# Kernel tuning notes

Hardware: AMD Instinct MI355X
Metric: run time of the kernel (lower is better)

## Reference

```python
import jax, jax.numpy as jnp
import numpy as np

D_MODEL = 768
N_LAYER = 8
EXPAND = 2
D_INNER = EXPAND * D_MODEL          # 1536
HEADDIM = 64
NHEADS = D_INNER // HEADDIM         # 24
D_STATE = 128
D_CONV = 4
NGROUPS = 1
CONV_DIM = D_INNER + 2 * NGROUPS * D_STATE      # 1792
D_IN_PROJ = 2 * D_INNER + 2 * NGROUPS * D_STATE + NHEADS  # 3352
DIM_INP = 6
DIM_OUT = 5
BATCH = 4
SEQ = 2048
EPS = 1e-5


def rmsnorm(x, w):
    return x * jax.lax.rsqrt(jnp.mean(x * x, axis=-1, keepdims=True) + EPS) * w


def setup_inputs() -> dict:
    key = jax.random.key(0)
    ks = jax.random.split(key, 12)
    nrm = lambda k, shape, s=0.02: jax.random.normal(k, shape, jnp.float32) * s
    x = jax.random.normal(ks[0], (BATCH, SEQ, DIM_INP), jnp.float32)
    y = jax.random.normal(ks[1], (BATCH, SEQ, DIM_OUT), jnp.float32)
    W_emb = nrm(ks[2], (D_MODEL, DIM_INP))
    b_emb = jnp.zeros((D_MODEL,), jnp.float32)
    # stacked per-layer Mamba2 params
    W_in = nrm(ks[3], (N_LAYER, D_IN_PROJ, D_MODEL))
    conv_w = nrm(ks[4], (N_LAYER, CONV_DIM, D_CONV), 0.2)
    conv_b = jnp.zeros((N_LAYER, CONV_DIM), jnp.float32)
    dt0 = jax.random.uniform(ks[5], (N_LAYER, NHEADS), jnp.float32, 1e-3, 1e-1)
    dt_bias = jnp.log(jnp.expm1(dt0))  # inverse softplus of target dt
    A_log = jnp.log(jax.random.uniform(ks[6], (N_LAYER, NHEADS), jnp.float32, 1.0, 16.0))
    Dp = jnp.ones((N_LAYER, NHEADS), jnp.float32)
    norm_w = jnp.ones((N_LAYER, D_INNER), jnp.float32)     # gated RMSNorm inside Mamba2
    W_out = nrm(ks[7], (N_LAYER, D_MODEL, D_INNER))
    block_norm_w = jnp.ones((N_LAYER, D_MODEL), jnp.float32)  # prenorm RMSNorm per block
    norm_f_w = jnp.ones((D_MODEL,), jnp.float32)
    W_head = nrm(ks[8], (DIM_OUT, D_MODEL))
    return dict(x=x, y=y, W_emb=W_emb, b_emb=b_emb, W_in=W_in, conv_w=conv_w,
                conv_b=conv_b, dt_bias=dt_bias, A_log=A_log, Dp=Dp, norm_w=norm_w,
                W_out=W_out, block_norm_w=block_norm_w, norm_f_w=norm_f_w, W_head=W_head)


def _mamba2(u, W_in_l, conv_w_l, conv_b_l, dt_bias_l, A_log_l, D_l, norm_w_l, W_out_l):
    B, L, _ = u.shape
    zxbcdt = jnp.einsum('bld,ed->ble', u, W_in_l)  # [B,L,D_IN_PROJ]
    z = zxbcdt[..., :D_INNER]
    xBC = zxbcdt[..., D_INNER:D_INNER + CONV_DIM]
    dt = jax.nn.softplus(zxbcdt[..., D_INNER + CONV_DIM:] + dt_bias_l)  # [B,L,H]
    # causal depthwise conv1d, kernel D_CONV
    xp = jnp.pad(xBC, ((0, 0), (D_CONV - 1, 0), (0, 0)))
    xBC = sum(xp[:, k:k + L, :] * conv_w_l[:, k] for k in range(D_CONV)) + conv_b_l
    xBC = jax.nn.silu(xBC)
    xh = xBC[..., :D_INNER].reshape(B, L, NHEADS, HEADDIM)
    Bm = xBC[..., D_INNER:D_INNER + D_STATE]   # [B,L,N] (ngroups=1)
    Cm = xBC[..., D_INNER + D_STATE:]          # [B,L,N]
    A = -jnp.exp(A_log_l)                       # [H]
    decay = jnp.exp(dt * A)                     # [B,L,H]
    dtx = dt[..., None] * xh                    # [B,L,H,P]

    def step(h, inp):
        dec_t, dtx_t, B_t, C_t = inp            # [B,H],[B,H,P],[B,N],[B,N]
        h = h * dec_t[..., None, None] + dtx_t[..., None] * B_t[:, None, None, :]
        y_t = jnp.einsum('bhpn,bn->bhp', h, C_t)
        return h, y_t

    h0 = jnp.zeros((B, NHEADS, HEADDIM, D_STATE), u.dtype)
    _, ys = jax.lax.scan(step, h0, (decay.transpose(1, 0, 2), dtx.transpose(1, 0, 2, 3),
                                    Bm.transpose(1, 0, 2), Cm.transpose(1, 0, 2)))
    ys = ys.transpose(1, 0, 2, 3) + xh * D_l[None, None, :, None]  # skip term D*x
    yf = ys.reshape(B, L, D_INNER)
    yf = rmsnorm(yf * jax.nn.silu(z), norm_w_l)  # gated RMSNorm (norm_before_gate=False)
    return jnp.einsum('bld,ed->ble', yf, W_out_l)


def _forward(x, W_emb, b_emb, W_in, conv_w, conv_b, dt_bias, A_log, Dp, norm_w,
             W_out, block_norm_w, norm_f_w, W_head):
    h = jnp.einsum('bli,di->bld', x, W_emb) + b_emb
    res = jnp.zeros_like(h)

    def layer_step(carry, lp):
        h, res = carry
        Wi, cw, cb, dtb, Al, Dl, nw, Wo, bnw = lp
        res = h + res
        hn = rmsnorm(res, bnw)
        h = _mamba2(hn, Wi, cw, cb, dtb, Al, Dl, nw, Wo)
        return (h, res), None

    (h, res), _ = jax.lax.scan(layer_step, (h, res),
                               (W_in, conv_w, conv_b, dt_bias, A_log, Dp, norm_w, W_out, block_norm_w))
    res = h + res
    hn = rmsnorm(res, norm_f_w)
    return jnp.einsum('bld,od->blo', hn, W_head)


def reference(x, y, W_emb, b_emb, W_in, conv_w, conv_b, dt_bias, A_log, Dp, norm_w,
              W_out, block_norm_w, norm_f_w, W_head):
    out = _forward(x, W_emb, b_emb, W_in, conv_w, conv_b, dt_bias, A_log, Dp, norm_w,
                   W_out, block_norm_w, norm_f_w, W_head)
    loss = jnp.mean((out - y) ** 2)
    return out, loss
```

## Files before the change

### kernel.cpp

```cpp
#include <hip/hip_runtime.h>
#include <hip/hip_bf16.h>
#include <math.h>

#define BATCH 4
#define SEQ 2048
#define DMODEL 768
#define NLAYER 8
#define DINNER 1536
#define HEADDIM 64
#define NHEADS 24
#define DSTATE 128
#define CONVDIM 1792
#define DINPROJ 3352
#define NPAD 3456
#define NPADW 3584
#define ROWS (BATCH*SEQ)
#define EPS 1e-5f
#define QCH 128
#define NCH (SEQ/QCH)

typedef __bf16 bf16;
typedef bf16 bf16x8 __attribute__((ext_vector_type(8)));
typedef bf16 bf16x4 __attribute__((ext_vector_type(4)));
typedef float f32x4 __attribute__((ext_vector_type(4)));

#define GLD(src, dst) __builtin_amdgcn_global_load_lds( \
    (const __attribute__((address_space(1))) void*)(src), \
    (__attribute__((address_space(3))) void*)(dst), 16, 0, 0)

__device__ __forceinline__ void bar_sync() {
    asm volatile("" ::: "memory");
    __builtin_amdgcn_s_barrier();
    asm volatile("" ::: "memory");
}

__device__ __forceinline__ float fsilu(float x) { return x / (1.f + __expf(-x)); }

__global__ void k_embed(const float* __restrict__ x, const float* __restrict__ We,
                        const float* __restrict__ be, float* __restrict__ res) {
    int idx = blockIdx.x * 256 + threadIdx.x;
    int d = idx % DMODEL; int bl = idx / DMODEL;
    float acc = be[d];
#pragma unroll
    for (int i = 0; i < 6; ++i) acc += x[bl * 6 + i] * We[d * 6 + i];
    res[idx] = acc;
}

__global__ __launch_bounds__(256) void k_rmsnorm(const float* __restrict__ res,
                                                 const float* __restrict__ w,
                                                 bf16* __restrict__ out) {
    __shared__ float sm[4];
    int r = blockIdx.x, tid = threadIdx.x;
    float v[3]; float ss = 0.f;
#pragma unroll
    for (int k = 0; k < 3; ++k) {
        int d = tid + k * 256;
        float t = res[r * DMODEL + d];
        v[k] = t; ss += t * t;
    }
#pragma unroll
    for (int off = 32; off; off >>= 1) ss += __shfl_down(ss, off, 64);
    if ((tid & 63) == 0) sm[tid >> 6] = ss;
    __syncthreads();
    float tot = sm[0] + sm[1] + sm[2] + sm[3];
    float sc = rsqrtf(tot / (float)DMODEL + EPS);
#pragma unroll
    for (int k = 0; k < 3; ++k) {
        int d = tid + k * 256;
        out[r * DMODEL + d] = (bf16)(v[k] * sc * w[d]);
    }
}

__global__ void k_cvt_in(const float* __restrict__ src, bf16* __restrict__ dst) {
    int idx = blockIdx.x * 256 + threadIdx.x;
    int l = idx / (NPADW * DMODEL);
    int rem = idx % (NPADW * DMODEL);
    int n = rem / DMODEL;
    int d = rem % DMODEL;
    dst[idx] = (n < DINPROJ) ? (bf16)src[(long)l * DINPROJ * DMODEL + n * DMODEL + d] : (bf16)0.f;
}
__global__ void k_cvt_out(const float* __restrict__ src, bf16* __restrict__ dst) {
    int idx = blockIdx.x * 256 + threadIdx.x;
    dst[idx] = (bf16)src[idx];
}

template <typename OT, int BM, int BN, int TH, bool ACC>
__global__ __launch_bounds__(TH) void k_gemm(const bf16* __restrict__ A, const bf16* __restrict__ B,
                                             OT* __restrict__ C, int K, int ldc, int Nact) {
    constexpr int NW  = TH / 64;
    constexpr int nWn = (BN / 64 < 4) ? BN / 64 : 4;
    constexpr int nWm = NW / nWn;
    constexpr int WMR = BM / nWm;
    constexpr int MI  = WMR / 16;
    constexpr int NI  = 4;
    constexpr int RG  = TH / 8;
    constexpr int AG  = BM / RG;
    constexpr int BG  = BN / RG;
    __shared__ bf16 As[2][BM * 64];
    __shared__ bf16 Bs[2][BN * 64];
    const int tid = threadIdx.x;
    const int lane = tid & 63;
    const int w = tid >> 6;
    const int wm = w / nWn, wn = w % nWn;
    const long rowA0 = (long)blockIdx.x * BM;
    const long rowB0 = (long)blockIdx.y * BN;
    const int srow = tid >> 3;
    const int scol = ((tid & 7) ^ (srow & 7)) * 8;
    const bf16* Ab = A + rowA0 * K + scol;
    const bf16* Bb = B + rowB0 * K + scol;

    f32x4 acc[MI][NI];
    const f32x4 vz = {0.f, 0.f, 0.f, 0.f};
#pragma unroll
    for (int mi = 0; mi < MI; ++mi)
#pragma unroll
        for (int ni = 0; ni < NI; ++ni) acc[mi][ni] = vz;

    auto stage = [&](int buf, int kt) {
#pragma unroll
        for (int j = 0; j < AG; ++j)
            GLD(Ab + (long)(j * RG + srow) * K + kt, &As[buf][(j * TH + w * 64) * 8]);
#pragma unroll
        for (int j = 0; j < BG; ++j)
            GLD(Bb + (long)(j * RG + srow) * K + kt, &Bs[buf][(j * TH + w * 64) * 8]);
    };
    auto waitv = [&]() {
        if constexpr (AG + BG == 8) asm volatile("s_waitcnt vmcnt(8)" ::: "memory");
        else                        asm volatile("s_waitcnt vmcnt(6)" ::: "memory");
    };
    auto compute = [&](int buf) {
        const char* AsB = (const char*)As[buf];
        const char* BsB = (const char*)Bs[buf];
#pragma unroll
        for (int s = 0; s < 2; ++s) {
            bf16x8 af[MI], bfr[NI];
#pragma unroll
            for (int mi = 0; mi < MI; ++mi) {
                int r = wm * WMR + mi * 16 + (lane & 15);
                af[mi] = *(const bf16x8*)(AsB + r * 128 + ((s * 64 + (lane >> 4) * 16) ^ ((r & 7) << 4)));
            }
#pragma unroll
            for (int ni = 0; ni < NI; ++ni) {
                int r = wn * 64 + ni * 16 + (lane & 15);
                bfr[ni] = *(const bf16x8*)(BsB + r * 128 + ((s * 64 + (lane >> 4) * 16) ^ ((r & 7) << 4)));
            }
#pragma unroll
            for (int mi = 0; mi < MI; ++mi)
#pragma unroll
                for (int ni = 0; ni < NI; ++ni)
                    acc[mi][ni] = __builtin_amdgcn_mfma_f32_16x16x32_bf16(af[mi], bfr[ni], acc[mi][ni], 0, 0, 0);
        }
    };

    stage(0, 0);
    stage(1, 64);
    int cur = 0;
    for (int kt = 128; kt < K; kt += 64) {
        waitv();
        bar_sync();
        compute(cur);
        bar_sync();
        stage(cur, kt);
        cur ^= 1;
    }
    waitv();
    bar_sync();
    compute(cur);
    asm volatile("s_waitcnt vmcnt(0)" ::: "memory");
    bar_sync();
    compute(cur ^ 1);

    const int crow = (lane >> 4) * 4;
    const int ccol = lane & 15;
#pragma unroll
    for (int mi = 0; mi < MI; ++mi)
#pragma unroll
        for (int ni = 0; ni < NI; ++ni) {
            long r0 = rowA0 + wm * WMR + mi * 16 + crow;
            long c0 = rowB0 + wn * 64 + ni * 16 + ccol;
            if ((int)c0 < Nact) {
#pragma unroll
                for (int j = 0; j < 4; ++j) {
                    if constexpr (ACC) C[(r0 + j) * ldc + c0] += (OT)acc[mi][ni][j];
                    else               C[(r0 + j) * ldc + c0]  = (OT)acc[mi][ni][j];
                }
            }
        }
}

__global__ void k_convBC(const bf16* __restrict__ zx, const float* __restrict__ cw,
                         const float* __restrict__ cb, bf16* __restrict__ bc) {
    int idx = blockIdx.x * 256 + threadIdx.x;
    int c8 = idx & 31; int blt = idx >> 5;
    int t = blt % SEQ;
    int ch = DINNER + c8 * 8;
    long bbase = (long)(blt - t) * NPAD;
    float cwa[8][4];
#pragma unroll
    for (int j = 0; j < 8; ++j) {
        float4 tv = *(const float4*)(cw + (ch + j) * 4);
        cwa[j][0] = tv.x; cwa[j][1] = tv.y; cwa[j][2] = tv.z; cwa[j][3] = tv.w;
    }
    float acc[8];
#pragma unroll
    for (int j = 0; j < 8; ++j) acc[j] = cb[ch + j];
#pragma unroll
    for (int k = 0; k < 4; ++k) {
        int tt = t + k - 3;
        if (tt >= 0) {
            bf16x8 v = *(const bf16x8*)(zx + bbase + (long)tt * NPAD + DINNER + ch);
#pragma unroll
            for (int j = 0; j < 8; ++j) acc[j] += (float)v[j] * cwa[j][k];
        }
    }
    bf16x8 o;
#pragma unroll
    for (int j = 0; j < 8; ++j) o[j] = (bf16)fsilu(acc[j]);
    *(bf16x8*)(bc + (long)blt * 256 + c8 * 8) = o;
}

__global__ __launch_bounds__(256) void k_prepL(const bf16* __restrict__ zx, const bf16* __restrict__ bc,
                                               const float* __restrict__ cw_l, const float* __restrict__ cb_l,
                                               const float* __restrict__ dt_bias_l,
                                               const float* __restrict__ Alog,
                                               float* __restrict__ Sarr, float* __restrict__ dtc,
                                               float* __restrict__ Pcb,
                                               bf16* __restrict__ XT, bf16* __restrict__ Lbuf) {
    __shared__ float S_lds[128], wl_lds[128], wtot[2];
    __shared__ bf16 Xs[136 * 64];
    __shared__ bf16 Xw[64 * 128];
    __shared__ bf16 Bt[128 * 128];
    int blk = blockIdx.x;
    int b = blk / (NHEADS * NCH);
    int r = blk % (NHEADS * NCH);
    int h = r / NCH;
    int c = r % NCH;
    int tid = threadIdx.x, lane = tid & 63, wid = tid >> 6;
    long brow0 = (long)b * SEQ + c * QCH;
#pragma unroll
    for (int i = 0; i < 5; ++i) {
        int base = i * 256 + wid * 64;
        if (base < 1048) {
            int idx = base + lane;
            long g = brow0 - 3 + (idx >> 3);
            if (g < 0) g = 0;
            if (g > (long)ROWS - 1) g = (long)ROWS - 1;
            GLD(zx + g * NPAD + DINNER + h * HEADDIM + (idx & 7) * 8,
                (char*)Xs + (long)base * 16);
        }
    }
    float ps = 0.f, dtv = 0.f;
    if (tid < 128) {
        float raw = (float)zx[(brow0 + tid) * NPAD + DINNER + CONVDIM + h] + dt_bias_l[h];
        dtv = (raw > 15.f) ? raw : log1pf(__expf(raw));
        float Ah = -__expf(Alog[h]);
        ps = dtv * Ah;
#pragma unroll
        for (int off = 1; off < 64; off <<= 1) {
            float o = __shfl_up(ps, off, 64);
            if ((tid & 63) >= off) ps += o;
        }
        if ((tid & 63) == 63) wtot[tid >> 6] = ps;
    }
    __syncthreads();
    if (tid < 128) {
        if (tid >= 64) ps += wtot[0];
        S_lds[tid] = ps;
    }
    __syncthreads();
    float Sl = S_lds[127];
    if (tid < 128) {
        wl_lds[tid] = __expf(Sl - ps) * dtv;
        Sarr[blk * QCH + tid] = ps;
        dtc[blk * QCH + tid] = dtv;
        if (tid == 127) Pcb[blk] = __expf(Sl);
    }
    __syncthreads();
    {
        int p = tid >> 2, q = tid & 3;
        float4 cwv = *(const float4*)(cw_l + (h * HEADDIM + p) * 4);
        float cbv = cb_l[h * HEADDIM + p];
        float cwa[4] = {cwv.x, cwv.y, cwv.z, cwv.w};
        char* xtb = (char*)XT + (((long)blk) << 14);
#pragma unroll
        for (int ub = 0; ub < 4; ++ub) {
            int u0 = q * 32 + ub * 8;
            bf16x8 vx, vw;
#pragma unroll
            for (int k = 0; k < 8; ++k) {
                int u = u0 + k;
                float a = cbv;
#pragma unroll
                for (int tt = 0; tt < 4; ++tt) {
                    if (c > 0 || u + tt >= 3)
                        a += (float)Xs[(u + tt) * 64 + p] * cwa[tt];
                }
                bf16 xb = (bf16)fsilu(a);
                vx[k] = xb;
                vw[k] = (bf16)((float)xb * wl_lds[u]);
            }
            long off = (long)((p * 256 + u0 * 2) ^ ((p & 7) << 4));
            *(bf16x8*)(xtb + off) = vx;
            *(bf16x8*)((char*)Xw + off) = vw;
        }
    }
#pragma unroll
    for (int nb = 0; nb < 2; ++nb) {
        __syncthreads();
#pragma unroll
        for (int i = 0; i < 4; ++i) {
            int idx = i * 256 + tid;
            GLD(bc + (brow0 + (idx >> 3)) * 256 + nb * 64 + (idx & 7) * 8,
                (char*)Xs + (i * 256 + wid * 64) * 16);
        }
        __syncthreads();
        int nl = tid >> 2, q = tid & 3;
        int n = nb * 64 + nl;
#pragma unroll
        for (int ub = 0; ub < 4; ++ub) {
            int u0 = q * 32 + ub * 8;
            bf16x8 v;
#pragma unroll
            for (int k = 0; k < 8; ++k) v[k] = Xs[(u0 + k) * 64 + nl];
            long off = (long)((n * 256 + u0 * 2) ^ ((n & 7) << 4));
            *(bf16x8*)((char*)Bt + off) = v;
        }
    }
    __syncthreads();
    f32x4 acc[4][2];
    const f32x4 vz = {0.f, 0.f, 0.f, 0.f};
#pragma unroll
    for (int mi = 0; mi < 4; ++mi)
#pragma unroll
        for (int ni = 0; ni < 2; ++ni) acc[mi][ni] = vz;
    const char* XwB = (const char*)Xw;
    const char* BtB = (const char*)Bt;
    __builtin_amdgcn_s_setprio(1);
#pragma unroll
    for (int ks = 0; ks < 4; ++ks) {
        bf16x8 af[4], bfr[2];
#pragma unroll
        for (int mi = 0; mi < 4; ++mi) {
            int pp = mi * 16 + (lane & 15);
            af[mi] = *(const bf16x8*)(XwB + ((pp * 256 + ks * 64 + (lane >> 4) * 16) ^ ((pp & 7) << 4)));
        }
#pragma unroll
        for (int ni = 0; ni < 2; ++ni) {
            int n = wid * 32 + ni * 16 + (lane & 15);
            bfr[ni] = *(const bf16x8*)(BtB + ((n * 256 + ks * 64 + (lane >> 4) * 16) ^ ((n & 7) << 4)));
        }
#pragma unroll
        for (int mi = 0; mi < 4; ++mi)
#pragma unroll
            for (int ni = 0; ni < 2; ++ni)
                acc[mi][ni] = __builtin_amdgcn_mfma_f32_16x16x32_bf16(af[mi], bfr[ni], acc[mi][ni], 0, 0, 0);
    }
    __builtin_amdgcn_s_setprio(0);
    char* lb = (char*)Lbuf + (((long)blk) << 14);
#pragma unroll
    for (int mi = 0; mi < 4; ++mi)
#pragma unroll
        for (int ni = 0; ni < 2; ++ni)
#pragma unroll
            for (int j = 0; j < 4; ++j) {
                int pp = mi * 16 + (lane >> 4) * 4 + j;
                int n = wid * 32 + ni * 16 + (lane & 15);
                *(bf16*)(lb + ((pp * 256 + n * 2) ^ ((pp & 7) << 4))) = (bf16)acc[mi][ni][j];
            }
}

__global__ __launch_bounds__(256) void k_scanB(bf16* __restrict__ Lbuf, const float* __restrict__ Pc) {
    int bh = blockIdx.x >> 2;
    int q = blockIdx.x & 3;
    int off = (q * 256 + threadIdx.x) * 8;
    long base = ((long)bh * NCH) << 13;
    float s[8] = {0.f};
#pragma unroll
    for (int c = 0; c < NCH; ++c) {
        bf16* p = Lbuf + base + ((long)c << 13) + off;
        bf16x8 L = *(bf16x8*)p;
        bf16x8 I;
#pragma unroll
        for (int k = 0; k < 8; ++k) I[k] = (bf16)s[k];
        float P = Pc[bh * NCH + c];
#pragma unroll
        for (int k = 0; k < 8; ++k) s[k] = P * s[k] + (float)L[k];
        *(bf16x8*)p = I;
    }
}

__global__ __launch_bounds__(512) void k_chunkY(const bf16* __restrict__ bc,
                                                const float* __restrict__ Sarr, const float* __restrict__ dtc,
                                                const float* __restrict__ Dp,
                                                const bf16* __restrict__ XT, const bf16* __restrict__ Lbuf,
                                                bf16* __restrict__ ysb) {
    __shared__ bf16 Cs[128 * 128];
    __shared__ bf16 Bs[128 * 128];
    __shared__ bf16 Xts[64 * 128];
    __shared__ bf16 Is[64 * 128];
    __shared__ float S_lds[128], dt_lds[128];
    int blk = blockIdx.x;
    int b = blk / (NHEADS * NCH);
    int r = blk % (NHEADS * NCH);
    int h = r / NCH;
    int c = r % NCH;
    int tid = threadIdx.x, lane = tid & 63, wid = tid >> 6;
    long brow0 = (long)b * SEQ + c * QCH;
    const char* bcB = (const char*)bc;
#pragma unroll
    for (int i = 0; i < 4; ++i) {
        int trow = i * 32 + wid * 4 + (lane >> 4);
        int blk16 = lane & 15;
        const char* rp = bcB + (brow0 + trow) * 512;
        int sb = (blk16 ^ (trow & 7)) << 4;
        GLD(rp + 256 + sb, (char*)Cs + (i * 32 + wid * 4) * 256);
        GLD(rp + sb,       (char*)Bs + (i * 32 + wid * 4) * 256);
    }
    const char* xt = (const char*)XT + (((long)blk) << 14);
    const char* ib = (const char*)Lbuf + (((long)blk) << 14);
#pragma unroll
    for (int i = 0; i < 2; ++i) {
        GLD(xt + (long)(i * 512 + tid) * 16, (char*)Xts + (i * 512 + wid * 64) * 16);
        GLD(ib + (long)(i * 512 + tid) * 16, (char*)Is + (i * 512 + wid * 64) * 16);
    }
    if (tid < 128) { S_lds[tid] = Sarr[blk * QCH + tid]; dt_lds[tid] = dtc[blk * QCH + tid]; }
    float Dh = Dp[h];
    asm volatile("s_waitcnt vmcnt(4) lgkmcnt(0)" ::: "memory");
    bar_sync();
    const char* CsB = (const char*)Cs;
    char* BsB = (char*)Bs;
    const char* IsB = (const char*)Is;
    const char* XtB = (const char*)Xts;
    const f32x4 vz = {0.f, 0.f, 0.f, 0.f};
    int wmG = wid >> 2, wnG = wid & 3;
    f32x4 accg[4][2];
#pragma unroll
    for (int mi = 0; mi < 4; ++mi)
#pragma unroll
        for (int ni = 0; ni < 2; ++ni) accg[mi][ni] = vz;
#pragma unroll
    for (int ks = 0; ks < 4; ++ks) {
        bf16x8 af[4], bfr[2];
#pragma unroll
        for (int mi = 0; mi < 4; ++mi) {
            int t = wmG * 64 + mi * 16 + (lane & 15);
            af[mi] = *(const bf16x8*)(CsB + ((t * 256 + ks * 64 + (lane >> 4) * 16) ^ ((t & 7) << 4)));
        }
#pragma unroll
        for (int ni = 0; ni < 2; ++ni) {
            int u = wnG * 32 + ni * 16 + (lane & 15);
            bfr[ni] = *(const bf16x8*)(BsB + ((u * 256 + ks * 64 + (lane >> 4) * 16) ^ ((u & 7) << 4)));
        }
#pragma unroll
        for (int mi = 0; mi < 4; ++mi)
#pragma unroll
            for (int ni = 0; ni < 2; ++ni)
                accg[mi][ni] = __builtin_amdgcn_mfma_f32_16x16x32_bf16(af[mi], bfr[ni], accg[mi][ni], 0, 0, 0);
    }
    bar_sync();
#pragma unroll
    for (int mi = 0; mi < 4; ++mi) {
#pragma unroll
        for (int j = 0; j < 4; ++j) {
            int t = wmG * 64 + mi * 16 + (lane >> 4) * 4 + j;
            float St = S_lds[t];
#pragma unroll
            for (int ni = 0; ni < 2; ++ni) {
                int u = wnG * 32 + ni * 16 + (lane & 15);
                float v = 0.f;
                if (u <= t) v = accg[mi][ni][j] * __expf(St - S_lds[u]) * dt_lds[u];
                *(bf16*)(BsB + ((t * 256 + u * 2) ^ ((t & 7) << 4))) = (bf16)v;
            }
        }
    }
    asm volatile("s_waitcnt vmcnt(0) lgkmcnt(0)" ::: "memory");
    bar_sync();
    int wmY = wid >> 1, wnY = wid & 1;
    f32x4 accy[2][2];
#pragma unroll
    for (int mi = 0; mi < 2; ++mi)
#pragma unroll
        for (int ni = 0; ni < 2; ++ni) accy[mi][ni] = vz;
#pragma unroll
    for (int ks = 0; ks < 4; ++ks) {
        bf16x8 af[2], bfr[2];
#pragma unroll
        for (int mi = 0; mi < 2; ++mi) {
            int t = wmY * 32 + mi * 16 + (lane & 15);
            af[mi] = *(const bf16x8*)(CsB + ((t * 256 + ks * 64 + (lane >> 4) * 16) ^ ((t & 7) << 4)));
        }
#pragma unroll
        for (int ni = 0; ni < 2; ++ni) {
            int pp = wnY * 32 + ni * 16 + (lane & 15);
            bfr[ni] = *(const bf16x8*)(IsB + ((pp * 256 + ks * 64 + (lane >> 4) * 16) ^ ((pp & 7) << 4)));
        }
#pragma unroll
        for (int mi = 0; mi < 2; ++mi)
#pragma unroll
            for (int ni = 0; ni < 2; ++ni)
                accy[mi][ni] = __builtin_amdgcn_mfma_f32_16x16x32_bf16(af[mi], bfr[ni], accy[mi][ni], 0, 0, 0);
    }
#pragma unroll
    for (int mi = 0; mi < 2; ++mi)
#pragma unroll
        for (int j = 0; j < 4; ++j) {
            int t = wmY * 32 + mi * 16 + (lane >> 4) * 4 + j;
            float e = __expf(S_lds[t]);
#pragma unroll
            for (int ni = 0; ni < 2; ++ni) accy[mi][ni][j] *= e;
        }
#pragma unroll
    for (int ks = 0; ks < 4; ++ks) {
        bf16x8 af[2], bfr[2];
#pragma unroll
        for (int mi = 0; mi < 2; ++mi) {
            int t = wmY * 32 + mi * 16 + (lane & 15);
            af[mi] = *(const bf16x8*)(BsB + ((t * 256 + ks * 64 + (lane >> 4) * 16) ^ ((t & 7) << 4)));
        }
#pragma unroll
        for (int ni = 0; ni < 2; ++ni) {
            int pp = wnY * 32 + ni * 16 + (lane & 15);
            bfr[ni] = *(const bf16x8*)(XtB + ((pp * 256 + ks * 64 + (lane >> 4) * 16) ^ ((pp & 7) << 4)));
        }
#pragma unroll
        for (int mi = 0; mi < 2; ++mi)
#pragma unroll
            for (int ni = 0; ni < 2; ++ni)
                accy[mi][ni] = __builtin_amdgcn_mfma_f32_16x16x32_bf16(af[mi], bfr[ni], accy[mi][ni], 0, 0, 0);
    }
#pragma unroll
    for (int mi = 0; mi < 2; ++mi)
#pragma unroll
        for (int ni = 0; ni < 2; ++ni)
#pragma unroll
            for (int j = 0; j < 4; ++j) {
                int t = wmY * 32 + mi * 16 + (lane >> 4) * 4 + j;
                int pp = wnY * 32 + ni * 16 + (lane & 15);
                float xv = (float)*(const bf16*)(XtB + ((pp * 256 + t * 2) ^ ((pp & 7) << 4)));
                ysb[(brow0 + t) * DINNER + h * HEADDIM + pp] = (bf16)(accy[mi][ni][j] + Dh * xv);
            }
}

__global__ __launch_bounds__(256) void k_gated(const bf16* __restrict__ ys, const bf16* __restrict__ zx,
                                               const float* __restrict__ w, bf16* __restrict__ out) {
    __shared__ float sm[4];
    int r = blockIdx.x, tid = threadIdx.x;
    float v[6]; float ss = 0.f;
#pragma unroll
    for (int k = 0; k < 6; ++k) {
        int d = tid + k * 256;
        float z = (float)zx[(long)r * NPAD + d];
        float t = (float)ys[(long)r * DINNER + d] * fsilu(z);
        v[k] = t; ss += t * t;
    }
#pragma unroll
    for (int off = 32; off; off >>= 1) ss += __shfl_down(ss, off, 64);
    if ((tid & 63) == 0) sm[tid >> 6] = ss;
    __syncthreads();
    float tot = sm[0] + sm[1] + sm[2] + sm[3];
    float sc = rsqrtf(tot / (float)DINNER + EPS);
#pragma unroll
    for (int k = 0; k < 6; ++k) {
        int d = tid + k * 256;
        out[(long)r * DINNER + d] = (bf16)(v[k] * sc * w[d]);
    }
}

__global__ __launch_bounds__(256) void k_head(const bf16* __restrict__ hn, const float* __restrict__ Wh,
                                              const float* __restrict__ y, float* __restrict__ out,
                                              float* __restrict__ loss) {
    __shared__ float sl[4];
    int tid = threadIdx.x, lane = tid & 63, wid = tid >> 6;
    float wv[5][12];
#pragma unroll
    for (int o = 0; o < 5; ++o)
#pragma unroll
        for (int j = 0; j < 12; ++j) wv[o][j] = Wh[o * DMODEL + lane * 12 + j];
    float lsum = 0.f;
#pragma unroll
    for (int rr = 0; rr < 8; ++rr) {
        long r = (long)blockIdx.x * 32 + wid * 8 + rr;
        const bf16* hp = hn + r * DMODEL + lane * 12;
        float hv[12];
#pragma unroll
        for (int q = 0; q < 3; ++q) {
            bf16x4 v4 = *(const bf16x4*)(hp + q * 4);
#pragma unroll
            for (int j = 0; j < 4; ++j) hv[q * 4 + j] = (float)v4[j];
        }
        float acc[5];
#pragma unroll
        for (int o = 0; o < 5; ++o) {
            float a = 0.f;
#pragma unroll
            for (int j = 0; j < 12; ++j) a += hv[j] * wv[o][j];
            acc[o] = a;
        }
#pragma unroll
        for (int o = 0; o < 5; ++o)
#pragma unroll
            for (int m = 32; m; m >>= 1) acc[o] += __shfl_xor(acc[o], m, 64);
        if (lane == 0) {
#pragma unroll
            for (int o = 0; o < 5; ++o) {
                out[r * 5 + o] = acc[o];
                float d = acc[o] - y[r * 5 + o];
                lsum += d * d;
            }
        }
    }
    if (lane == 0) sl[wid] = lsum;
    __syncthreads();
    if (tid == 0) atomicAdd(loss, (sl[0] + sl[1] + sl[2] + sl[3]) * (1.f / ((float)ROWS * 5.f)));
}

extern "C" void kernel_launch(void* const* d_in, const int* in_sizes, int n_in,
                              void* d_out, int out_size, void* d_ws, size_t ws_size,
                              hipStream_t stream) {
    const float* x      = (const float*)d_in[0];
    const float* y      = (const float*)d_in[1];
    const float* W_emb  = (const float*)d_in[2];
    const float* b_emb  = (const float*)d_in[3];
    const float* W_in   = (const float*)d_in[4];
    const float* conv_w = (const float*)d_in[5];
    const float* conv_b = (const float*)d_in[6];
    const float* dt_bias= (const float*)d_in[7];
    const float* A_log  = (const float*)d_in[8];
    const float* Dp     = (const float*)d_in[9];
    const float* norm_w = (const float*)d_in[10];
    const float* W_out  = (const float*)d_in[11];
    const float* bnw    = (const float*)d_in[12];
    const float* nfw    = (const float*)d_in[13];
    const float* W_head = (const float*)d_in[14];

    char* ws = (char*)d_ws;
    float* res  = (float*)ws;  ws += (size_t)ROWS * DMODEL * 4;
    bf16*  Lbuf = (bf16*)ws;   ws += (size_t)BATCH * NHEADS * NCH * 8192 * 2;
    bf16*  hnb  = (bf16*)ws;   ws += (size_t)ROWS * DMODEL * 2;
    bf16*  zx   = (bf16*)ws;   ws += (size_t)ROWS * NPAD * 2;
    bf16*  bc   = (bf16*)ws;   ws += (size_t)ROWS * 256 * 2;
    bf16*  ysb  = (bf16*)ws;   ws += (size_t)ROWS * DINNER * 2;
    bf16*  yfb  = (bf16*)ws;   ws += (size_t)ROWS * DINNER * 2;
    bf16*  Wib  = (bf16*)ws;   ws += (size_t)NLAYER * NPADW * DMODEL * 2;
    bf16*  Wob  = (bf16*)ws;   ws += (size_t)NLAYER * DMODEL * DINNER * 2;
    float* Pcb  = (float*)ws;  ws += (size_t)BATCH * NHEADS * NCH * 4;
    float* Sarr = (float*)ws;  ws += (size_t)BATCH * NHEADS * NCH * QCH * 4;
    float* dtc  = (float*)ws;  ws += (size_t)BATCH * NHEADS * NCH * QCH * 4;
    bf16*  XT   = (bf16*)ws;   ws += (size_t)BATCH * NHEADS * NCH * 8192 * 2;

    float* out_p  = (float*)d_out;
    float* loss_p = out_p + (size_t)ROWS * 5;

    hipMemsetAsync(loss_p, 0, 4, stream);
    k_embed<<<ROWS * DMODEL / 256, 256, 0, stream>>>(x, W_emb, b_emb, res);
    k_cvt_in<<<NLAYER * NPADW * DMODEL / 256, 256, 0, stream>>>(W_in, Wib);
    k_cvt_out<<<NLAYER * DMODEL * DINNER / 256, 256, 0, stream>>>(W_out, Wob);

    const int NBHC = BATCH * NHEADS * NCH;
    for (int l = 0; l < NLAYER; ++l) {
        const float* cw_l = conv_w + (size_t)l * CONVDIM * 4;
        const float* cb_l = conv_b + (size_t)l * CONVDIM;
        k_rmsnorm<<<ROWS, 256, 0, stream>>>(res, bnw + l * DMODEL, hnb);
        dim3 g1(ROWS / 256, NPADW / 256);
        k_gemm<bf16, 256, 256, 512, false><<<g1, 512, 0, stream>>>(hnb, Wib + (size_t)l * NPADW * DMODEL, zx, DMODEL, NPAD, NPAD);
        k_convBC<<<ROWS * 32 / 256, 256, 0, stream>>>(zx, cw_l, cb_l, bc);
        k_prepL<<<NBHC, 256, 0, stream>>>(zx, bc, cw_l, cb_l, dt_bias + l * NHEADS, A_log + l * NHEADS,
                                          Sarr, dtc, Pcb, XT, Lbuf);
        k_scanB<<<BATCH * NHEADS * 4, 256, 0, stream>>>(Lbuf, Pcb);
        k_chunkY<<<NBHC, 512, 0, stream>>>(bc, Sarr, dtc, Dp + l * NHEADS, XT, Lbuf, ysb);
        k_gated<<<ROWS, 256, 0, stream>>>(ysb, zx, norm_w + l * DINNER, yfb);
        dim3 g2(ROWS / 128, DMODEL / 64);
        k_gemm<float, 128, 64, 256, true><<<g2, 256, 0, stream>>>(yfb, Wob + (size_t)l * DMODEL * DINNER, res, DINNER, DMODEL, DMODEL);
    }

    k_rmsnorm<<<ROWS, 256, 0, stream>>>(res, nfw, hnb);
    k_head<<<256, 256, 0, stream>>>(hnb, W_head, y, out_p, loss_p);
}
```

Measured before the change: 1.741 ms.

## Overlap next-tile global loads with second half of MFMA work in GEMM

Restructures the GEMM main loop so each k-tile's LDS fragments are read in two halves. The second half's fragments go into registers before the barrier, so the global-to-LDS stage for tile t+2 is issued while the second half of the MFMAs runs. The goal is to hide global load latency behind matrix math instead of serialising compute and staging. The cost is more fragment registers held live, which may raise register pressure, and MI must be even.

```diff
diff --git a/kernel.cpp b/kernel.cpp
--- a/kernel.cpp
+++ b/kernel.cpp
@@ -92,6 +92,7 @@
     constexpr int nWm = NW / nWn;
     constexpr int WMR = BM / nWm;
     constexpr int MI  = WMR / 16;
+    constexpr int MH  = MI / 2;
     constexpr int NI  = 4;
     constexpr int RG  = TH / 8;
     constexpr int AG  = BM / RG;
@@ -128,47 +129,73 @@
         if constexpr (AG + BG == 8) asm volatile("s_waitcnt vmcnt(8)" ::: "memory");
         else                        asm volatile("s_waitcnt vmcnt(6)" ::: "memory");
     };
-    auto compute = [&](int buf) {
+
+    bf16x8 bfr[NI][2];
+    bf16x8 af[MH][2];
+    auto rd_bfr = [&](int buf) {
+        const char* BsB = (const char*)Bs[buf];
+#pragma unroll
+        for (int ni = 0; ni < NI; ++ni)
+#pragma unroll
+            for (int ks = 0; ks < 2; ++ks) {
+                int r = wn * 64 + ni * 16 + (lane & 15);
+                bfr[ni][ks] = *(const bf16x8*)(BsB + r * 128 + ((ks * 64 + (lane >> 4) * 16) ^ ((r & 7) << 4)));
+            }
+    };
+    auto rd_af = [&](int buf, int m0) {
         const char* AsB = (const char*)As[buf];
-        const char* BsB = (const char*)Bs[buf];
-#pragma unroll
-        for (int s = 0; s < 2; ++s) {
-            bf16x8 af[MI], bfr[NI];
-#pragma unroll
-            for (int mi = 0; mi < MI; ++mi) {
-                int r = wm * WMR + mi * 16 + (lane & 15);
-                af[mi] = *(const bf16x8*)(AsB + r * 128 + ((s * 64 + (lane >> 4) * 16) ^ ((r & 7) << 4)));
+#pragma unroll
+        for (int mi = 0; mi < MH; ++mi)
+#pragma unroll
+            for (int ks = 0; ks < 2; ++ks) {
+                int r = wm * WMR + (m0 + mi) * 16 + (lane & 15);
+                af[mi][ks] = *(const bf16x8*)(AsB + r * 128 + ((ks * 64 + (lane >> 4) * 16) ^ ((r & 7) << 4)));
             }
-#pragma unroll
-            for (int ni = 0; ni < NI; ++ni) {
-                int r = wn * 64 + ni * 16 + (lane & 15);
-                bfr[ni] = *(const bf16x8*)(BsB + r * 128 + ((s * 64 + (lane >> 4) * 16) ^ ((r & 7) << 4)));
-            }
-#pragma unroll
-            for (int mi = 0; mi < MI; ++mi)
-#pragma unroll
-                for (int ni = 0; ni < NI; ++ni)
-                    acc[mi][ni] = __builtin_amdgcn_mfma_f32_16x16x32_bf16(af[mi], bfr[ni], acc[mi][ni], 0, 0, 0);
-        }
     };
-
+    auto do_half = [&](int m0) {
+#pragma unroll
+        for (int mi = 0; mi < MH; ++mi)
+#pragma unroll
+            for (int ni = 0; ni < NI; ++ni)
+#pragma unroll
+                for (int ks = 0; ks < 2; ++ks)
+                    acc[m0 + mi][ni] = __builtin_amdgcn_mfma_f32_16x16x32_bf16(af[mi][ks], bfr[ni][ks], acc[m0 + mi][ni], 0, 0, 0);
+    };
+
+    const int NT = K / 64;
     stage(0, 0);
     stage(1, 64);
-    int cur = 0;
-    for (int kt = 128; kt < K; kt += 64) {
+    for (int t = 0; t < NT - 2; ++t) {
         waitv();
         bar_sync();
-        compute(cur);
+        rd_bfr(t & 1);
+        rd_af(t & 1, 0);
+        do_half(0);
+        rd_af(t & 1, MH);
+        asm volatile("s_waitcnt lgkmcnt(0)" ::: "memory");
         bar_sync();
-        stage(cur, kt);
-        cur ^= 1;
-    }
-    waitv();
-    bar_sync();
-    compute(cur);
-    asm volatile("s_waitcnt vmcnt(0)" ::: "memory");
-    bar_sync();
-    compute(cur ^ 1);
+        stage(t & 1, (t + 2) * 64);
+        __builtin_amdgcn_sched_barrier(0);
+        do_half(MH);
+    }
+    {
+        waitv();
+        bar_sync();
+        rd_bfr((NT - 2) & 1);
+        rd_af((NT - 2) & 1, 0);
+        do_half(0);
+        rd_af((NT - 2) & 1, MH);
+        do_half(MH);
+    }
+    {
+        asm volatile("s_waitcnt vmcnt(0)" ::: "memory");
+        bar_sync();
+        rd_bfr((NT - 1) & 1);
+        rd_af((NT - 1) & 1, 0);
+        do_half(0);
+        rd_af((NT - 1) & 1, MH);
+        do_half(MH);
+    }
 
     const int crow = (lane >> 4) * 4;
     const int ccol = lane & 15;
```

Result: no change. 1.732 ms (-0.5%).
